# Kernel optimization log

Measured on AMD Instinct MI355X. Metric: run time of the kernel, lower is better.

## Reference

```python
import jax, jax.numpy as jnp
import numpy as np

NUM_EMBEDDINGS = 512
EMBEDDING_DIM = 64
COMMITMENT_COST = 0.25


def setup_inputs() -> dict:
    key = jax.random.key(0)
    k1, k2 = jax.random.split(key)
    x = jax.random.normal(k1, (32, 64, 64, 64), dtype=jnp.float32)  # [B, C=D, H, W]
    # torch init: uniform(-1/K, 1/K)
    w = jax.random.uniform(k2, (NUM_EMBEDDINGS, EMBEDDING_DIM), dtype=jnp.float32,
                           minval=-1.0 / NUM_EMBEDDINGS, maxval=1.0 / NUM_EMBEDDINGS)
    return {"x": x, "w": w}


def reference(x, w):
    # [B, C, H, W] -> [B, H, W, C]
    xt = jnp.transpose(x, (0, 2, 3, 1))
    flat = xt.reshape(-1, EMBEDDING_DIM)  # [N, D]
    # squared L2 distances to each codebook vector: [N, K]
    distances = (jnp.sum(flat * flat, axis=1, keepdims=True)
                 + jnp.sum(w * w, axis=1)
                 - 2.0 * flat @ w.T)
    idx = jnp.argmin(distances, axis=1)  # [N]
    encodings = jax.nn.one_hot(idx, NUM_EMBEDDINGS, dtype=x.dtype)  # [N, K]
    quantized = w[idx].reshape(xt.shape)  # gather == one_hot @ w
    e_latent_loss = jnp.mean((jax.lax.stop_gradient(quantized) - xt) ** 2)
    q_latent_loss = jnp.mean((quantized - jax.lax.stop_gradient(xt)) ** 2)
    quant_loss = q_latent_loss + COMMITMENT_COST * e_latent_loss
    # straight-through estimator
    quantized_st = xt + jax.lax.stop_gradient(quantized - xt)
    quantized_out = jnp.transpose(quantized_st, (0, 3, 1, 2))  # back to [B, C, H, W]
    avg_probs = jnp.mean(encodings, axis=0)
    perplexity = jnp.exp(-jnp.sum(avg_probs * jnp.log(avg_probs + 1e-10)))
    return quantized_out, quant_loss, encodings, perplexity
```

## Files before the change

### kernel.cpp

```cpp
#include <hip/hip_runtime.h>
#include <math.h>

#define TB        256
#define POSB      256
#define NPOS      131072
#define KCODES    512
#define DIM       64
#define HW        4096
#define LOSS_OFF  8388608ull
#define ENC_OFF   8388609ull
#define PERP_OFF  75497473ull
#define TILE_DW   (POSB * KCODES)
#define NF4       ((TILE_DW - 4) / 4)
#define TAU       2.0e-4f

typedef __attribute__((ext_vector_type(8))) short bf16x8;
typedef __attribute__((ext_vector_type(4))) float f32x4;

__device__ __forceinline__ float tree8(float r0, float r1, float r2, float r3,
                                       float r4, float r5, float r6, float r7) {
    return __fadd_rn(__fadd_rn(__fadd_rn(r0, r1), __fadd_rn(r2, r3)),
                     __fadd_rn(__fadd_rn(r4, r5), __fadd_rn(r6, r7)));
}

extern "C" __global__ __launch_bounds__(512)
void vq_prep(const float* __restrict__ w, float* __restrict__ ww,
             int* __restrict__ counts, float* __restrict__ lossAcc,
             unsigned short* __restrict__ wfrag)
{
    const int t = threadIdx.x;
    if (blockIdx.x < 32) {
        const int ct = blockIdx.x;
        if (t < 256) {
            const int part = t >> 7, q = (t >> 6) & 1, lf = t & 63;
            const int n = lf & 15, k = ct * 16 + n;
            const float* wk = w + (size_t)k * DIM;
            unsigned short v8[8];
            #pragma unroll
            for (int j8 = 0; j8 < 8; ++j8) {
                const int d = q * 32 + ((lf >> 4) << 3) + j8;
                float v = wk[d];
                unsigned int hb = __float_as_uint(v) & 0xFFFF0000u;
                if (part == 0) {
                    v8[j8] = (unsigned short)(hb >> 16);
                } else {
                    float rr = v - __uint_as_float(hb);
                    v8[j8] = (unsigned short)(__float_as_uint(rr) >> 16);
                }
            }
            bf16x8* dst = reinterpret_cast<bf16x8*>(wfrag);
            dst[((part * 32 + ct) * 2 + q) * 64 + lf] =
                *reinterpret_cast<const bf16x8*>(v8);
        }
    } else {
        const int k = t;
        const float* wk = w + (size_t)k * DIM;
        float r[8];
        #pragma unroll
        for (int i = 0; i < 8; ++i) {
            #pragma unroll
            for (int j = 0; j < 8; ++j) {
                float v = wk[i * 8 + j];
                float pp = __fmul_rn(v, v);
                r[j] = (i == 0) ? pp : __fadd_rn(r[j], pp);
            }
        }
        ww[k] = tree8(r[0], r[1], r[2], r[3], r[4], r[5], r[6], r[7]);
        counts[k] = 0;
        if (k == 0) *lossAcc = 0.0f;
    }
}

#define FRAG(PART, CT, Q) wf[((((PART) * 32 + (CT)) * 2 + (Q)) * 64) + l]

#define TILE6(PT, B0, B1, B2, B3, WWK)                                        \
    acc = (f32x4){(WWK), (WWK), (WWK), (WWK)};                                \
    acc = __builtin_amdgcn_mfma_f32_16x16x32_bf16(aL0[PT], B0, acc, 0, 0, 0); \
    acc = __builtin_amdgcn_mfma_f32_16x16x32_bf16(aH0[PT], B2, acc, 0, 0, 0); \
    acc = __builtin_amdgcn_mfma_f32_16x16x32_bf16(aH0[PT], B0, acc, 0, 0, 0); \
    acc = __builtin_amdgcn_mfma_f32_16x16x32_bf16(aL1[PT], B1, acc, 0, 0, 0); \
    acc = __builtin_amdgcn_mfma_f32_16x16x32_bf16(aH1[PT], B3, acc, 0, 0, 0); \
    acc = __builtin_amdgcn_mfma_f32_16x16x32_bf16(aH1[PT], B1, acc, 0, 0, 0);

extern "C" __global__ __launch_bounds__(TB)
__attribute__((amdgpu_waves_per_eu(2, 8)))
void vq_main(const float* __restrict__ x, const float* __restrict__ w,
             const float* __restrict__ ww, float* __restrict__ out,
             int* __restrict__ counts, float* __restrict__ lossAcc,
             const unsigned short* __restrict__ wfrag)
{
    __shared__ __align__(16) float xtile[DIM][POSB + 1];
    __shared__ float wwlds[KCODES];
    __shared__ int   hcount[KCODES];
    __shared__ int   ccount[POSB];
    __shared__ int   clist[POSB * 4];
    __shared__ int   bestkL[POSB];

    const int tid = threadIdx.x;
    const int l   = tid & 63;
    const int wv  = tid >> 6;
    const int n0  = blockIdx.x * POSB;
    const int b   = n0 >> 12;
    const int hw0 = n0 & 4095;

    hcount[tid]      = 0;
    hcount[tid + TB] = 0;
    ccount[tid]      = 0;
    wwlds[tid]       = ww[tid];
    wwlds[tid + TB]  = ww[tid + TB];

    const float* xb = x + ((size_t)b * DIM) * HW + hw0;
    #pragma unroll
    for (int it = 0; it < 64; ++it) {
        const int idx = it * TB + tid;
        const int d = idx >> 8, ps = idx & 255;
        xtile[d][ps] = xb[(size_t)d * HW + ps];
    }
    __syncthreads();

    bf16x8 aH0[4], aH1[4], aL0[4], aL1[4];
    #pragma unroll
    for (int pt = 0; pt < 4; ++pt) {
        const int arow = (wv * 4 + pt) * 16 + (l & 15);
        #pragma unroll
        for (int q = 0; q < 2; ++q) {
            #pragma unroll
            for (int j8 = 0; j8 < 8; ++j8) {
                const int d = q * 32 + ((l >> 4) << 3) + j8;
                float v = xtile[d][arow];
                float m2 = -(v + v);
                unsigned int hb = __float_as_uint(m2) & 0xFFFF0000u;
                float rr = m2 - __uint_as_float(hb);
                short hs = (short)(hb >> 16);
                short ls = (short)(__float_as_uint(rr) >> 16);
                if (q == 0) { aH0[pt][j8] = hs; aL0[pt][j8] = ls; }
                else        { aH1[pt][j8] = hs; aL1[pt][j8] = ls; }
            }
        }
    }

    const bf16x8* wf = reinterpret_cast<const bf16x8*>(wfrag);
    const int rloc = (l >> 4) << 2;

    const size_t T0 = ENC_OFF + (size_t)blockIdx.x * TILE_DW;
    float4* zs4 = reinterpret_cast<float4*>(out + T0 + 3);
    const float4 zero4 = make_float4(0.0f, 0.0f, 0.0f, 0.0f);
    if (tid < 3)  out[T0 + tid] = 0.0f;
    if (tid == 3) out[T0 + (TILE_DW - 1)] = 0.0f;

    float rmin[4][4];
    #pragma unroll
    for (int pt = 0; pt < 4; ++pt)
        #pragma unroll
        for (int i = 0; i < 4; ++i) rmin[pt][i] = INFINITY;
    {
        bf16x8 c0 = FRAG(0, 0, 0), c1 = FRAG(0, 0, 1);
        bf16x8 c2 = FRAG(1, 0, 0), c3 = FRAG(1, 0, 1);
        float wa = wwlds[(l & 15)];
        f32x4 acc;
        #pragma unroll 1
        for (int ct = 0; ct < 32; ++ct) {
            const int nt = (ct + 1) & 31;
            bf16x8 p0 = FRAG(0, nt, 0), p1 = FRAG(0, nt, 1);
            bf16x8 p2 = FRAG(1, nt, 0), p3 = FRAG(1, nt, 1);
            float wb = wwlds[nt * 16 + (l & 15)];
            #pragma unroll
            for (int pt = 0; pt < 4; ++pt) {
                TILE6(pt, c0, c1, c2, c3, wa)
                #pragma unroll
                for (int i = 0; i < 4; ++i)
                    rmin[pt][i] = fminf(rmin[pt][i], acc[i]);
            }
            {
                const int mb = ct * (TB * 2) + tid;
                zs4[mb]              = zero4;
                zs4[mb + TB]         = zero4;
                const int mb2 = (TB * 64) + ct * (TB * 2) + tid;
                zs4[mb2]             = zero4;
                zs4[mb2 + TB]        = zero4;
            }
            c0 = p0; c1 = p1; c2 = p2; c3 = p3; wa = wb;
        }
    }
    float thr[4][4];
    #pragma unroll
    for (int pt = 0; pt < 4; ++pt) {
        #pragma unroll
        for (int mm = 1; mm < 16; mm <<= 1)
            #pragma unroll
            for (int i = 0; i < 4; ++i)
                rmin[pt][i] = fminf(rmin[pt][i], __shfl_xor(rmin[pt][i], mm));
        #pragma unroll
        for (int i = 0; i < 4; ++i) thr[pt][i] = rmin[pt][i] + TAU;
    }

    {
        bf16x8 c0 = FRAG(0, 0, 0), c1 = FRAG(0, 0, 1);
        bf16x8 c2 = FRAG(1, 0, 0), c3 = FRAG(1, 0, 1);
        float wa = wwlds[(l & 15)];
        f32x4 acc;
        #pragma unroll 1
        for (int ct = 0; ct < 32; ++ct) {
            const int nt = (ct + 1) & 31;
            bf16x8 p0 = FRAG(0, nt, 0), p1 = FRAG(0, nt, 1);
            bf16x8 p2 = FRAG(1, nt, 0), p3 = FRAG(1, nt, 1);
            float wb = wwlds[nt * 16 + (l & 15)];
            #pragma unroll
            for (int pt = 0; pt < 4; ++pt) {
                TILE6(pt, c0, c1, c2, c3, wa)
                const int prow = (wv * 4 + pt) * 16 + rloc;
                #pragma unroll
                for (int i = 0; i < 4; ++i) {
                    if (acc[i] <= thr[pt][i]) {
                        int s = atomicAdd(&ccount[prow + i], 1);
                        if (s < 4) clist[(prow + i) * 4 + s] = ct * 16 + (l & 15);
                    }
                }
            }
            {
                const int mb = 16384 + ct * (TB * 2) + tid;
                zs4[mb]       = zero4;
                if (mb + TB < NF4) zs4[mb + TB] = zero4;
                const int mb2 = 16384 + (TB * 64) + ct * (TB * 2) + tid;
                if (mb2 < NF4)      zs4[mb2]      = zero4;
                if (mb2 + TB < NF4) zs4[mb2 + TB] = zero4;
            }
            c0 = p0; c1 = p1; c2 = p2; c3 = p3; wa = wb;
        }
    }

    __syncthreads();

    {
        const int p = wv * 64 + l;
        const int cnt = ccount[p];
        int bk;
        if (cnt == 1) {
            bk = clist[p * 4 + 0];
        } else {
            float x2c[DIM];
            float r[8];
            #pragma unroll
            for (int d = 0; d < DIM; ++d) {
                float v = xtile[d][p];
                x2c[d] = v + v;
                float pp = __fmul_rn(v, v);
                r[d & 7] = (d < 8) ? pp : __fadd_rn(r[d & 7], pp);
            }
            const float A = tree8(r[0], r[1], r[2], r[3], r[4], r[5], r[6], r[7]);
            if (cnt <= 4) {
                float bd = INFINITY; int bk2 = KCODES;
                for (int c = 0; c < cnt; ++c) {
                    const int k = clist[p * 4 + c];
                    const float* wk = w + (size_t)k * DIM;
                    float s[8];
                    #pragma unroll
                    for (int i = 0; i < 8; ++i) {
                        #pragma unroll
                        for (int j = 0; j < 8; ++j) {
                            const int d = i * 8 + j;
                            float wvv = wk[d];
                            if (i == 0) s[j] = __fmul_rn(x2c[d], wvv);
                            else        s[j] = __fmaf_rn(x2c[d], wvv, s[j]);
                        }
                    }
                    float dot  = tree8(s[0], s[1], s[2], s[3], s[4], s[5], s[6], s[7]);
                    float dist = __fadd_rn(__fadd_rn(A, wwlds[k]), -dot);
                    if (dist < bd || (dist == bd && k < bk2)) { bd = dist; bk2 = k; }
                }
                bk = bk2;
            } else {
                float bd = INFINITY; int bk2 = 0;
                #pragma unroll 1
                for (int k = 0; k < KCODES; ++k) {
                    const float* wk = w + (size_t)k * DIM;
                    float s[8];
                    #pragma unroll
                    for (int i = 0; i < 8; ++i) {
                        #pragma unroll
                        for (int j = 0; j < 8; ++j) {
                            const int d = i * 8 + j;
                            float wvv = wk[d];
                            if (i == 0) s[j] = __fmul_rn(x2c[d], wvv);
                            else        s[j] = __fmaf_rn(x2c[d], wvv, s[j]);
                        }
                    }
                    float dot  = tree8(s[0], s[1], s[2], s[3], s[4], s[5], s[6], s[7]);
                    float dist = __fadd_rn(__fadd_rn(A, wwlds[k]), -dot);
                    if (dist < bd) { bd = dist; bk2 = k; }
                }
                bk = bk2;
            }
        }
        bestkL[p] = bk;
        out[ENC_OFF + (size_t)(n0 + p) * KCODES + bk] = 1.0f;
        atomicAdd(&hcount[bk], 1);
    }

    __syncthreads();

    {
        const int sp = tid;
        const int bk = bestkL[sp];
        const float4* wr = reinterpret_cast<const float4*>(w + (size_t)bk * DIM);
        float* qo = out + ((size_t)b * DIM) * HW + (hw0 + sp);
        float sse = 0.0f;
        #pragma unroll
        for (int c = 0; c < 16; ++c) {
            float4 qv = wr[c];
            const int ch = c * 4;
            qo[(size_t)(ch + 0) * HW] = qv.x;
            qo[(size_t)(ch + 1) * HW] = qv.y;
            qo[(size_t)(ch + 2) * HW] = qv.z;
            qo[(size_t)(ch + 3) * HW] = qv.w;
            float e0 = qv.x - xtile[ch + 0][sp]; sse = __fmaf_rn(e0, e0, sse);
            float e1 = qv.y - xtile[ch + 1][sp]; sse = __fmaf_rn(e1, e1, sse);
            float e2 = qv.z - xtile[ch + 2][sp]; sse = __fmaf_rn(e2, e2, sse);
            float e3 = qv.w - xtile[ch + 3][sp]; sse = __fmaf_rn(e3, e3, sse);
        }
        #pragma unroll
        for (int off = 32; off > 0; off >>= 1) sse += __shfl_down(sse, off);
        if (l == 0) atomicAdd(lossAcc, sse);
    }

    __syncthreads();

    {
        int c0 = hcount[tid];       if (c0) atomicAdd(&counts[tid], c0);
        int c1 = hcount[tid + TB];  if (c1) atomicAdd(&counts[tid + TB], c1);
    }
}

extern "C" __global__ __launch_bounds__(512)
void vq_finalize(const int* __restrict__ counts, const float* __restrict__ lossAcc,
                 float* __restrict__ out)
{
    __shared__ double sred[KCODES];
    const int t = threadIdx.x;
    double p = (double)counts[t] * (1.0 / (double)NPOS);
    sred[t] = -p * log(p + 1e-10);
    __syncthreads();
    for (int s = KCODES / 2; s > 0; s >>= 1) {
        if (t < s) sred[t] += sred[t + s];
        __syncthreads();
    }
    if (t == 0) {
        out[PERP_OFF] = (float)exp(sred[0]);
        out[LOSS_OFF] = 1.25f * (lossAcc[0] / 8388608.0f);
    }
}

extern "C" void kernel_launch(void* const* d_in, const int* in_sizes, int n_in,
                              void* d_out, int out_size, void* d_ws, size_t ws_size,
                              hipStream_t stream)
{
    const float* x = (const float*)d_in[0];
    const float* w = (const float*)d_in[1];
    float* out = (float*)d_out;

    float* ww              = (float*)d_ws;
    int*   counts          = (int*)((char*)d_ws + 2048);
    float* lossAcc         = (float*)((char*)d_ws + 4096);
    unsigned short* wfrag  = (unsigned short*)((char*)d_ws + 8192);

    vq_prep<<<33, 512, 0, stream>>>(w, ww, counts, lossAcc, wfrag);
    vq_main<<<NPOS / POSB, TB, 0, stream>>>(x, w, ww, out, counts,
                                            lossAcc, wfrag);
    vq_finalize<<<1, 512, 0, stream>>>(counts, lossAcc, out);
}
```

Baseline: 392.4 us.

## Write one-hot encodings in a single pass and deepen fragment prefetch

The zero-fill of the one-hot encoding tile, previously spread across the two distance-scan loops and followed by a scattered write of each 1.0, is replaced by one pass at the end of the block. That pass writes every float4 of the tile with the correct 0/1 values read from the per-position best-index table in shared memory. This removes the overlap of stores with the MFMA loops and the extra scattered write, but the encoding write is now serialized after compute. The codebook fragment prefetch in both scan loops is also deepened from one tile ahead to two, which raises register pressure.

```diff
diff --git a/kernel.cpp b/kernel.cpp
--- a/kernel.cpp
+++ b/kernel.cpp
@@ -13,6 +13,7 @@
 #define TILE_DW   (POSB * KCODES)
 #define NF4       ((TILE_DW - 4) / 4)
 #define TAU       2.0e-4f
+#define NBLK      (NPOS / POSB)
 
 typedef __attribute__((ext_vector_type(8))) short bf16x8;
 typedef __attribute__((ext_vector_type(4))) float f32x4;
@@ -142,12 +143,6 @@
     const bf16x8* wf = reinterpret_cast<const bf16x8*>(wfrag);
     const int rloc = (l >> 4) << 2;
 
-    const size_t T0 = ENC_OFF + (size_t)blockIdx.x * TILE_DW;
-    float4* zs4 = reinterpret_cast<float4*>(out + T0 + 3);
-    const float4 zero4 = make_float4(0.0f, 0.0f, 0.0f, 0.0f);
-    if (tid < 3)  out[T0 + tid] = 0.0f;
-    if (tid == 3) out[T0 + (TILE_DW - 1)] = 0.0f;
-
     float rmin[4][4];
     #pragma unroll
     for (int pt = 0; pt < 4; ++pt)
@@ -156,14 +151,17 @@
     {
         bf16x8 c0 = FRAG(0, 0, 0), c1 = FRAG(0, 0, 1);
         bf16x8 c2 = FRAG(1, 0, 0), c3 = FRAG(1, 0, 1);
+        bf16x8 d0 = FRAG(0, 1, 0), d1 = FRAG(0, 1, 1);
+        bf16x8 d2 = FRAG(1, 1, 0), d3 = FRAG(1, 1, 1);
         float wa = wwlds[(l & 15)];
+        float wbn = wwlds[16 + (l & 15)];
         f32x4 acc;
         #pragma unroll 1
         for (int ct = 0; ct < 32; ++ct) {
-            const int nt = (ct + 1) & 31;
-            bf16x8 p0 = FRAG(0, nt, 0), p1 = FRAG(0, nt, 1);
-            bf16x8 p2 = FRAG(1, nt, 0), p3 = FRAG(1, nt, 1);
-            float wb = wwlds[nt * 16 + (l & 15)];
+            const int ft = (ct + 2) & 31;
+            bf16x8 e0 = FRAG(0, ft, 0), e1 = FRAG(0, ft, 1);
+            bf16x8 e2 = FRAG(1, ft, 0), e3 = FRAG(1, ft, 1);
+            float wc = wwlds[ft * 16 + (l & 15)];
             #pragma unroll
             for (int pt = 0; pt < 4; ++pt) {
                 TILE6(pt, c0, c1, c2, c3, wa)
@@ -171,15 +169,8 @@
                 for (int i = 0; i < 4; ++i)
                     rmin[pt][i] = fminf(rmin[pt][i], acc[i]);
             }
-            {
-                const int mb = ct * (TB * 2) + tid;
-                zs4[mb]              = zero4;
-                zs4[mb + TB]         = zero4;
-                const int mb2 = (TB * 64) + ct * (TB * 2) + tid;
-                zs4[mb2]             = zero4;
-                zs4[mb2 + TB]        = zero4;
-            }
-            c0 = p0; c1 = p1; c2 = p2; c3 = p3; wa = wb;
+            c0 = d0; c1 = d1; c2 = d2; c3 = d3; wa = wbn;
+            d0 = e0; d1 = e1; d2 = e2; d3 = e3; wbn = wc;
         }
     }
     float thr[4][4];
@@ -197,14 +188,17 @@
     {
         bf16x8 c0 = FRAG(0, 0, 0), c1 = FRAG(0, 0, 1);
         bf16x8 c2 = FRAG(1, 0, 0), c3 = FRAG(1, 0, 1);
+        bf16x8 d0 = FRAG(0, 1, 0), d1 = FRAG(0, 1, 1);
+        bf16x8 d2 = FRAG(1, 1, 0), d3 = FRAG(1, 1, 1);
         float wa = wwlds[(l & 15)];
+        float wbn = wwlds[16 + (l & 15)];
         f32x4 acc;
         #pragma unroll 1
         for (int ct = 0; ct < 32; ++ct) {
-            const int nt = (ct + 1) & 31;
-            bf16x8 p0 = FRAG(0, nt, 0), p1 = FRAG(0, nt, 1);
-            bf16x8 p2 = FRAG(1, nt, 0), p3 = FRAG(1, nt, 1);
-            float wb = wwlds[nt * 16 + (l & 15)];
+            const int ft = (ct + 2) & 31;
+            bf16x8 e0 = FRAG(0, ft, 0), e1 = FRAG(0, ft, 1);
+            bf16x8 e2 = FRAG(1, ft, 0), e3 = FRAG(1, ft, 1);
+            float wc = wwlds[ft * 16 + (l & 15)];
             #pragma unroll
             for (int pt = 0; pt < 4; ++pt) {
                 TILE6(pt, c0, c1, c2, c3, wa)
@@ -217,15 +211,8 @@
                     }
                 }
             }
-            {
-                const int mb = 16384 + ct * (TB * 2) + tid;
-                zs4[mb]       = zero4;
-                if (mb + TB < NF4) zs4[mb + TB] = zero4;
-                const int mb2 = 16384 + (TB * 64) + ct * (TB * 2) + tid;
-                if (mb2 < NF4)      zs4[mb2]      = zero4;
-                if (mb2 + TB < NF4) zs4[mb2 + TB] = zero4;
-            }
-            c0 = p0; c1 = p1; c2 = p2; c3 = p3; wa = wb;
+            c0 = d0; c1 = d1; c2 = d2; c3 = d3; wa = wbn;
+            d0 = e0; d1 = e1; d2 = e2; d3 = e3; wbn = wc;
         }
     }
 
@@ -293,7 +280,6 @@
             }
         }
         bestkL[p] = bk;
-        out[ENC_OFF + (size_t)(n0 + p) * KCODES + bk] = 1.0f;
         atomicAdd(&hcount[bk], 1);
     }
 
@@ -323,7 +309,30 @@
         if (l == 0) atomicAdd(lossAcc, sse);
     }
 
-    __syncthreads();
+    {
+        const size_t T0 = ENC_OFF + (size_t)blockIdx.x * TILE_DW;
+        if (tid < 3)  out[T0 + tid] = (bestkL[0] == tid) ? 1.0f : 0.0f;
+        if (tid == 3) out[T0 + (TILE_DW - 1)] =
+                          (bestkL[POSB - 1] == (KCODES - 1)) ? 1.0f : 0.0f;
+        f32x4* zs4 = reinterpret_cast<f32x4*>(out + T0 + 3);
+        #pragma unroll 4
+        for (int it = 0; it < 128; ++it) {
+            const int m = it * TB + tid;
+            if (m < NF4) {
+                const int o0 = 3 + 4 * m;
+                const int pa = o0 >> 9,       ca = o0 & 511;
+                const int pb = (o0 + 1) >> 9, cb = (o0 + 1) & 511;
+                const int pc = (o0 + 2) >> 9, cc = (o0 + 2) & 511;
+                const int pd = (o0 + 3) >> 9, cd = (o0 + 3) & 511;
+                f32x4 v;
+                v.x = (bestkL[pa] == ca) ? 1.0f : 0.0f;
+                v.y = (bestkL[pb] == cb) ? 1.0f : 0.0f;
+                v.z = (bestkL[pc] == cc) ? 1.0f : 0.0f;
+                v.w = (bestkL[pd] == cd) ? 1.0f : 0.0f;
+                zs4[m] = v;
+            }
+        }
+    }
 
     {
         int c0 = hcount[tid];       if (c0) atomicAdd(&counts[tid], c0);
@@ -364,7 +373,6 @@
     unsigned short* wfrag  = (unsigned short*)((char*)d_ws + 8192);
 
     vq_prep<<<33, 512, 0, stream>>>(w, ww, counts, lossAcc, wfrag);
-    vq_main<<<NPOS / POSB, TB, 0, stream>>>(x, w, ww, out, counts,
-                                            lossAcc, wfrag);
+    vq_main<<<NBLK, TB, 0, stream>>>(x, w, ww, out, counts, lossAcc, wfrag);
     vq_finalize<<<1, 512, 0, stream>>>(counts, lossAcc, out);
 }
```

New measurement: 389.9 us. About the same (-0.6%).
